# Kernel optimization log

Hardware: AMD Instinct MI355X
Metric: run time of the kernel (lower is better)

## Reference

```python
import jax, jax.numpy as jnp
import numpy as np

B, S, D = 4, 4096, 2048
G, EPG = 4, 16          # num_groups, experts_per_group
E = G * EPG             # num_experts = 64
H = 64                  # complexity estimator hidden


def setup_inputs() -> dict:
    key = jax.random.key(0)
    ks = jax.random.split(key, 7)
    scale = 0.02
    return {
        "x": jax.random.normal(ks[0], (B, S, D), dtype=jnp.float32),
        "Wg": jax.random.normal(ks[1], (G, D), dtype=jnp.float32) * scale,
        "We": jax.random.normal(ks[2], (G, EPG, D), dtype=jnp.float32) * scale,
        "W1": jax.random.normal(ks[3], (H, D), dtype=jnp.float32) * scale,
        "b1": jax.random.normal(ks[4], (H,), dtype=jnp.float32) * scale,
        "W2": jax.random.normal(ks[5], (1, H), dtype=jnp.float32) * scale,
        "b2": jax.random.normal(ks[6], (1,), dtype=jnp.float32) * scale,
        "min_experts": 1,
        "max_experts": 2,
    }


def _router_forward(x, Wg, We, W1, b1, W2, b2, min_experts, max_experts):
    # complexity estimator: Linear -> ReLU -> Linear -> Sigmoid, squeeze(-1)
    h = jax.nn.relu(jnp.einsum("bsd,hd->bsh", x, W1) + b1)
    complexity = jax.nn.sigmoid(jnp.einsum("bsh,oh->bso", h, W2) + b2)[..., 0]  # [B,S]
    # torch: clamp((score * max_experts).int(), min, max); .int() truncates (floor for >=0)
    k = jnp.clip((complexity * max_experts).astype(jnp.int32), min_experts, max_experts)  # [B,S]

    # group routing
    group_logits = jnp.einsum("bsd,gd->bsg", x, Wg)          # [B,S,G]
    group_probs = jax.nn.softmax(group_logits, axis=-1)
    gidx = jnp.argmax(group_probs, axis=-1)                   # [B,S]

    # per-group expert logits for all groups, then pick the chosen group per token
    expert_logits_all = jnp.einsum("bsd,ged->bsge", x, We)    # [B,S,G,EPG]
    expert_logits = jnp.take_along_axis(
        expert_logits_all, gidx[:, :, None, None], axis=2
    )[:, :, 0, :]                                             # [B,S,EPG]
    expert_probs = jax.nn.softmax(expert_logits, axis=-1)     # [B,S,EPG]

    # per-token top-k (k in {1,2}); always take top-2, mask the 2nd when k==1
    topv, topi = jax.lax.top_k(expert_probs, max_experts)     # [B,S,2]
    use2 = (k >= 2).astype(topv.dtype)                        # [B,S]
    mask = jnp.stack([jnp.ones_like(use2), use2], axis=-1)    # [B,S,2]
    denom = jnp.sum(topv * mask, axis=-1, keepdims=True)
    norm_probs = topv * mask / denom                          # [B,S,2]

    flat_idx = gidx[:, :, None] * EPG + topi                  # [B,S,2] global expert ids
    oh = jax.nn.one_hot(flat_idx, E, dtype=x.dtype)           # [B,S,2,E]
    dispatch = jnp.sum(oh * mask[..., None], axis=2)          # [B,S,E]
    combine = jnp.sum(oh * norm_probs[..., None], axis=2)     # [B,S,E]

    # router_probs: group_prob[gidx] * expert_probs scattered into chosen group's slice
    gp_max = jnp.take_along_axis(group_probs, gidx[..., None], axis=-1)[..., 0]  # [B,S]
    oh_g = jax.nn.one_hot(gidx, G, dtype=x.dtype)             # [B,S,G]
    router_probs = (oh_g[..., :, None] * (gp_max[..., None] * expert_probs)[..., None, :]
                    ).reshape(x.shape[0], x.shape[1], E)      # [B,S,E]

    denom_tok = x.shape[0] * x.shape[1]
    router_prob_per_expert = jnp.sum(router_probs, axis=(0, 1)) / denom_tok
    expert_usage = jnp.sum(dispatch, axis=(0, 1)) / denom_tok
    aux_loss = jnp.sum(router_prob_per_expert * expert_usage) * E
    return dispatch, combine, router_probs, aux_loss


def reference(x, Wg, We, W1, b1, W2, b2, min_experts, max_experts):
    return _router_forward(x, Wg, We, W1, b1, W2, b2, min_experts, max_experts)
```

## Files before the change

### kernel.cpp

```cpp
#include <hip/hip_runtime.h>
#include <cmath>

#define T_TOKENS 16384
#define DIM 2048
#define NG 4
#define EPG 16
#define NE 64
#define NJ2 68
#define NT2 5
#define BM 64
#define BK 64
#define NITER (DIM / BK)
#define TAU 0.02f

#define XBUF_B 16384
#define WBUF_B 10240

typedef __attribute__((ext_vector_type(8))) short bf16x8;
typedef __attribute__((ext_vector_type(4))) float f32x4;

#define WF_FLOATS (64 * NT2 * 64 * 4)
#define SUM_OFF WF_FLOATS
#define CNT_OFF (SUM_OFF + 128)
#define LIST_OFF (CNT_OFF + 4)

static __device__ inline unsigned bf16rne(float x) {
    unsigned u = __float_as_uint(x);
    return (u + 0x7FFFu + ((u >> 16) & 1u)) >> 16;
}

#define GLOAD_LDS(gsrc, ldst) \
    __builtin_amdgcn_global_load_lds( \
        (const __attribute__((address_space(1))) void*)(gsrc), \
        (__attribute__((address_space(3))) void*)(ldst), 16, 0, 0)

__global__ void moe_prep(const float* __restrict__ Wg, const float* __restrict__ We,
                         float* __restrict__ ws, float* __restrict__ sums,
                         int* __restrict__ cnt) {
    int bid = blockIdx.x;
    int kstep = bid / NT2, nt = bid % NT2;
    int lane = threadIdx.x;
    if (bid == 0) {
        sums[lane] = 0.f; sums[64 + lane] = 0.f;
        if (lane == 0) *cnt = 0;
    }
    int row = nt * 16 + (lane & 15);
    int k0 = kstep * 32 + (lane >> 4) * 8;
    const float* src = nullptr;
    if (row < NG)            src = Wg + (size_t)row * DIM;
    else if (row < NJ2)      src = We + (size_t)(row - NG) * DIM;
    unsigned r0 = 0, r1 = 0, r2 = 0, r3 = 0;
    if (src) {
        r0 = bf16rne(src[k0 + 0]) | (bf16rne(src[k0 + 1]) << 16);
        r1 = bf16rne(src[k0 + 2]) | (bf16rne(src[k0 + 3]) << 16);
        r2 = bf16rne(src[k0 + 4]) | (bf16rne(src[k0 + 5]) << 16);
        r3 = bf16rne(src[k0 + 6]) | (bf16rne(src[k0 + 7]) << 16);
    }
    ((uint4*)ws)[(size_t)(kstep * NT2 + nt) * 64 + lane] = make_uint4(r0, r1, r2, r3);
}

__global__ __launch_bounds__(512, 2) void moe_fused(
    const float* __restrict__ x, const float* __restrict__ wfrag,
    float* __restrict__ out, float* __restrict__ sums,
    int* __restrict__ cnt, int4* __restrict__ list) {
    __shared__ __align__(16) char smem[2 * XBUF_B + 2 * WBUF_B];
    __shared__ float rp_s[BM * 17];
    __shared__ int   sc_e1[BM];
    __shared__ float s_usage[NE], s_rp[NE];

    const int tid = threadIdx.x;
    const int wave = tid >> 6, lane = tid & 63;
    const int l15 = lane & 15, lq = lane >> 4;
    const int T0 = blockIdx.x * BM;

    if (tid < NE) { s_usage[tid] = 0.f; s_rp[tid] = 0.f; }

    const uint4* wg = (const uint4*)wfrag;
    const int mt = wave & 3, nh = wave >> 2;
    const int ctok = mt * 16 + l15;
    const int csw = ctok & 7;

    f32x4 acc0 = (f32x4){0.f,0.f,0.f,0.f};
    f32x4 acc1 = (f32x4){0.f,0.f,0.f,0.f};
    f32x4 acc2 = (f32x4){0.f,0.f,0.f,0.f};

    auto stage = [&](int it) {
        char* xb = smem + (it & 1) * XBUF_B;
        char* wb = smem + 2 * XBUF_B + (it & 1) * WBUF_B;
        const int kf = it * BK;
        #pragma unroll
        for (int j = 0; j < 2; ++j) {
            const int tok = wave * 8 + j * 4 + (lane >> 4);
            const float* src = x + (size_t)(T0 + tok) * DIM + kf
                             + (((lane & 15) ^ (tok & 7)) << 2);
            GLOAD_LDS(src, xb + (wave * 8 + j * 4) * 256);
        }
        if (wave < NT2) {
            #pragma unroll
            for (int ks = 0; ks < 2; ++ks) {
                const int kstep = it * 2 + ks;
                GLOAD_LDS(wg + ((size_t)kstep * NT2 + wave) * 64 + lane,
                          wb + (ks * NT2 + wave) * 1024);
            }
        }
    };

    stage(0);
    #pragma unroll 1
    for (int it = 0; it < NITER; ++it) {
        __syncthreads();
        if (it + 1 < NITER) stage(it + 1);
        const char* xb = smem + (it & 1) * XBUF_B;
        const char* wb = smem + 2 * XBUF_B + (it & 1) * WBUF_B;
        #pragma unroll
        for (int ks = 0; ks < 2; ++ks) {
            const int u0 = ks * 8 + lq * 2;
            uint4 lo = *(const uint4*)(xb + ctok * 256 + ((u0 ^ csw) << 4));
            uint4 hi = *(const uint4*)(xb + ctok * 256 + (((u0 + 1) ^ csw) << 4));
            union { unsigned u[4]; bf16x8 v; } af;
            af.u[0] = (lo.x >> 16) | (lo.y & 0xFFFF0000u);
            af.u[1] = (lo.z >> 16) | (lo.w & 0xFFFF0000u);
            af.u[2] = (hi.x >> 16) | (hi.y & 0xFFFF0000u);
            af.u[3] = (hi.z >> 16) | (hi.w & 0xFFFF0000u);
            if (nh == 0) {
                bf16x8 b0 = *(const bf16x8*)(wb + (ks * NT2 + 0) * 1024 + lane * 16);
                bf16x8 b1 = *(const bf16x8*)(wb + (ks * NT2 + 1) * 1024 + lane * 16);
                bf16x8 b2 = *(const bf16x8*)(wb + (ks * NT2 + 2) * 1024 + lane * 16);
                acc0 = __builtin_amdgcn_mfma_f32_16x16x32_bf16(af.v, b0, acc0, 0, 0, 0);
                acc1 = __builtin_amdgcn_mfma_f32_16x16x32_bf16(af.v, b1, acc1, 0, 0, 0);
                acc2 = __builtin_amdgcn_mfma_f32_16x16x32_bf16(af.v, b2, acc2, 0, 0, 0);
            } else {
                bf16x8 b0 = *(const bf16x8*)(wb + (ks * NT2 + 3) * 1024 + lane * 16);
                bf16x8 b1 = *(const bf16x8*)(wb + (ks * NT2 + 4) * 1024 + lane * 16);
                acc0 = __builtin_amdgcn_mfma_f32_16x16x32_bf16(af.v, b0, acc0, 0, 0, 0);
                acc1 = __builtin_amdgcn_mfma_f32_16x16x32_bf16(af.v, b1, acc1, 0, 0, 0);
            }
        }
    }
    __syncthreads();

    float* slog = (float*)smem;
    #pragma unroll
    for (int r = 0; r < 4; ++r) {
        const int row = mt * 16 + lq * 4 + r;
        if (nh == 0) {
            slog[row * 81 + 0 * 16 + l15] = acc0[r];
            slog[row * 81 + 1 * 16 + l15] = acc1[r];
            slog[row * 81 + 2 * 16 + l15] = acc2[r];
        } else {
            slog[row * 81 + 3 * 16 + l15] = acc0[r];
            slog[row * 81 + 4 * 16 + l15] = acc1[r];
        }
    }
    __syncthreads();

    #pragma unroll
    for (int half = 0; half < 2; ++half) {
        const int t = (tid >> 4) + half * 32;
        const int q = tid & 15;
        const int tok = T0 + t;
        const float* o = slog + t * 81;

        float gl0 = o[0], gl1 = o[1], gl2 = o[2], gl3 = o[3];
        float gm = gl0; int gi = 0;
        if (gl1 > gm) { gm = gl1; gi = 1; }
        if (gl2 > gm) { gm = gl2; gi = 2; }
        if (gl3 > gm) { gm = gl3; gi = 3; }
        float g2 = -INFINITY;
        if (gi != 0 && gl0 > g2) g2 = gl0;
        if (gi != 1 && gl1 > g2) g2 = gl1;
        if (gi != 2 && gl2 > g2) g2 = gl2;
        if (gi != 3 && gl3 > g2) g2 = gl3;
        bool flagG = (gm - g2) < TAU;
        float gsum = expf(gl0 - gm) + expf(gl1 - gm) + expf(gl2 - gm) + expf(gl3 - gm);
        float gp = 1.f / gsum;

        float el = o[NG + gi * EPG + q];
        float v1v = el; int i1 = q;
        #pragma unroll
        for (int off = 8; off; off >>= 1) {
            float ov = __shfl_xor(v1v, off, 16);
            int   oi = __shfl_xor(i1, off, 16);
            if (ov > v1v || (ov == v1v && oi < i1)) { v1v = ov; i1 = oi; }
        }
        float v2v = (q == i1) ? -INFINITY : el;
        #pragma unroll
        for (int off = 8; off; off >>= 1)
            v2v = fmaxf(v2v, __shfl_xor(v2v, off, 16));
        bool flagE = (v1v - v2v) < TAU;

        float ep = expf(el - v1v);
        float es = ep;
        #pragma unroll
        for (int off = 8; off; off >>= 1) es += __shfl_xor(es, off, 16);
        float inv = 1.f / es;
        rp_s[t * 17 + q] = gp * ep * inv;

        if (q == 0) {
            sc_e1[t] = gi * EPG + i1;
            if (flagG || flagE) {
                int p = atomicAdd(cnt, 1);
                list[p] = make_int4(tok, 0, 0, 0);
            }
        }
    }
    __syncthreads();

    float* outD = out;
    float* outC = out + (size_t)T_TOKENS * NE;
    float* outR = out + (size_t)2 * T_TOKENS * NE;
    for (int idx = tid; idx < BM * NE; idx += 512) {
        int t = idx >> 6, e = idx & 63;
        int e1i = sc_e1[t];
        int gi = e1i >> 4;
        float disp = (e == e1i) ? 1.f : 0.f;
        float rpv  = ((e >> 4) == gi) ? rp_s[t * 17 + (e & 15)] : 0.f;
        size_t ob = (size_t)(T0 + t) * NE + e;
        outD[ob] = disp; outC[ob] = disp; outR[ob] = rpv;
        atomicAdd(&s_usage[e], disp);
        atomicAdd(&s_rp[e], rpv);
    }
    __syncthreads();
    if (tid < NE) {
        atomicAdd(&sums[tid], s_usage[tid]);
        atomicAdd(&sums[NE + tid], s_rp[tid]);
    }
}

__global__ __launch_bounds__(256, 4) void moe_fix(
    const float* __restrict__ x, const float* __restrict__ Wg,
    const float* __restrict__ We, float* __restrict__ out,
    float* __restrict__ sums, const int* __restrict__ cnt,
    const int4* __restrict__ list) {
    __shared__ float gl_s[NG];
    __shared__ float el_s[EPG];
    __shared__ float rp_row[EPG];
    __shared__ int   s_gi, s_e1;
    __shared__ float s_gp;

    const int tid = threadIdx.x;
    const int wave = tid >> 6, lane = tid & 63;
    const int n = *cnt;

    for (int i = blockIdx.x; i < n; i += gridDim.x) {
        const int tok = list[i].x;
        const float* xrow = x + (size_t)tok * DIM;
        float xr[32];
        #pragma unroll
        for (int m = 0; m < 32; ++m) xr[m] = xrow[lane + m * 64];

        auto dotf = [&](const float* w) -> float {
            float s = 0.f;
            #pragma unroll
            for (int m = 0; m < 32; ++m) s = fmaf(xr[m], w[lane + m * 64], s);
            #pragma unroll
            for (int off = 32; off; off >>= 1) s += __shfl_xor(s, off, 64);
            return s;
        };

        {
            float g = dotf(Wg + (size_t)wave * DIM);
            if (lane == 0) gl_s[wave] = g;
        }
        __syncthreads();

        if (tid == 0) {
            float gm = -INFINITY; int gi = 0;
            #pragma unroll
            for (int g = 0; g < NG; ++g)
                if (gl_s[g] > gm) { gm = gl_s[g]; gi = g; }
            float gsum = 0.f;
            #pragma unroll
            for (int g = 0; g < NG; ++g) gsum += expf(gl_s[g] - gm);
            s_gp = 1.f / gsum;
            s_gi = gi;
        }
        __syncthreads();

        const int gi = s_gi;
        for (int j = wave; j < EPG; j += 4) {
            float e = dotf(We + (size_t)(gi * EPG + j) * DIM);
            if (lane == 0) el_s[j] = e;
        }
        __syncthreads();

        if (tid == 0) {
            float e1 = -INFINITY; int i1 = 0;
            #pragma unroll
            for (int j = 0; j < EPG; ++j)
                if (el_s[j] > e1) { e1 = el_s[j]; i1 = j; }
            float es = 0.f;
            #pragma unroll
            for (int j = 0; j < EPG; ++j) {
                float e = expf(el_s[j] - e1);
                rp_row[j] = e;
                es += e;
            }
            float sc = s_gp / es;
            #pragma unroll
            for (int j = 0; j < EPG; ++j) rp_row[j] *= sc;
            s_e1 = gi * EPG + i1;
        }
        __syncthreads();

        if (tid < NE) {
            const int e = tid;
            float newD = (e == s_e1) ? 1.f : 0.f;
            float newR = ((e >> 4) == gi) ? rp_row[e & 15] : 0.f;
            size_t ob = (size_t)tok * NE + e;
            float oldD = out[ob];
            float oldR = out[(size_t)2 * T_TOKENS * NE + ob];
            out[ob] = newD;
            out[(size_t)T_TOKENS * NE + ob] = newD;
            out[(size_t)2 * T_TOKENS * NE + ob] = newR;
            float dD = newD - oldD, dR = newR - oldR;
            if (dD != 0.f) atomicAdd(&sums[e], dD);
            if (dR != 0.f) atomicAdd(&sums[NE + e], dR);
        }
        __syncthreads();
    }
}

__global__ void moe_finalize(const float* __restrict__ sums, float* __restrict__ out) {
    int l = threadIdx.x;
    float v = sums[l] * sums[NE + l];
    #pragma unroll
    for (int off = 32; off; off >>= 1) v += __shfl_down(v, off, 64);
    if (l == 0) {
        float N = (float)T_TOKENS;
        out[(size_t)3 * T_TOKENS * NE] = v * (float)NE / (N * N);
    }
}

extern "C" void kernel_launch(void* const* d_in, const int* in_sizes, int n_in,
                              void* d_out, int out_size, void* d_ws, size_t ws_size,
                              hipStream_t stream) {
    const float* x  = (const float*)d_in[0];
    const float* Wg = (const float*)d_in[1];
    const float* We = (const float*)d_in[2];
    float* out = (float*)d_out;
    float* ws  = (float*)d_ws;

    float* wfrag = ws;
    float* sums  = ws + SUM_OFF;
    int*   cnt   = (int*)(ws + CNT_OFF);
    int4*  list  = (int4*)(ws + LIST_OFF);

    moe_prep<<<64 * NT2, 64, 0, stream>>>(Wg, We, wfrag, sums, cnt);
    moe_fused<<<T_TOKENS / BM, 512, 0, stream>>>(x, wfrag, out, sums, cnt, list);
    moe_fix<<<1024, 256, 0, stream>>>(x, Wg, We, out, sums, cnt, list);
    moe_finalize<<<1, 64, 0, stream>>>(sums, out);
}
```

Baseline: 79.59 us.

## Split GEMM along K into partial sums with separate epilogue kernel

Replaces the fused per-64-token GEMM+epilogue kernel with a split-K GEMM: 256-token tiles and 4 K-slices write partial logits to workspace. A new epilogue kernel sums the partials and does the softmax/top-k and output writes over 16-token blocks. The intent is larger tiles that reuse each weight fragment across two M tiles, with K-parallelism to fill the GPU. The cost is an extra launch and about 21 MB of partial-sum traffic to global memory.

```diff
diff --git a/kernel.cpp b/kernel.cpp
--- a/kernel.cpp
+++ b/kernel.cpp
@@ -8,19 +8,23 @@
 #define NE 64
 #define NJ2 68
 #define NT2 5
-#define BM 64
-#define BK 64
-#define NITER (DIM / BK)
+#define NJP2 80
+#define BM 256
+#define KS 4
+#define KSL (DIM / KS)
+#define NITER (KSL / 32)
 #define TAU 0.02f
 
-#define XBUF_B 16384
-#define WBUF_B 10240
+#define XBUF_B 32768
+#define WBUF_B 5120
 
 typedef __attribute__((ext_vector_type(8))) short bf16x8;
 typedef __attribute__((ext_vector_type(4))) float f32x4;
 
 #define WF_FLOATS (64 * NT2 * 64 * 4)
-#define SUM_OFF WF_FLOATS
+#define P_OFF WF_FLOATS
+#define P_FLOATS ((size_t)KS * T_TOKENS * NJP2)
+#define SUM_OFF (P_OFF + P_FLOATS)
 #define CNT_OFF (SUM_OFF + 128)
 #define LIST_OFF (CNT_OFF + 4)
 
@@ -47,8 +51,8 @@
     int row = nt * 16 + (lane & 15);
     int k0 = kstep * 32 + (lane >> 4) * 8;
     const float* src = nullptr;
-    if (row < NG)            src = Wg + (size_t)row * DIM;
-    else if (row < NJ2)      src = We + (size_t)(row - NG) * DIM;
+    if (row < NG)        src = Wg + (size_t)row * DIM;
+    else if (row < NJ2)  src = We + (size_t)(row - NG) * DIM;
     unsigned r0 = 0, r1 = 0, r2 = 0, r3 = 0;
     if (src) {
         r0 = bf16rne(src[k0 + 0]) | (bf16rne(src[k0 + 1]) << 16);
@@ -59,49 +63,47 @@
     ((uint4*)ws)[(size_t)(kstep * NT2 + nt) * 64 + lane] = make_uint4(r0, r1, r2, r3);
 }
 
-__global__ __launch_bounds__(512, 2) void moe_fused(
+__global__ __launch_bounds__(512, 1) void moe_gemm(
     const float* __restrict__ x, const float* __restrict__ wfrag,
-    float* __restrict__ out, float* __restrict__ sums,
-    int* __restrict__ cnt, int4* __restrict__ list) {
-    __shared__ __align__(16) char smem[2 * XBUF_B + 2 * WBUF_B];
-    __shared__ float rp_s[BM * 17];
-    __shared__ int   sc_e1[BM];
-    __shared__ float s_usage[NE], s_rp[NE];
-
+    float* __restrict__ part) {
+    __shared__ __align__(16) char xs[2][XBUF_B];
+    __shared__ __align__(16) char wsb[2][WBUF_B];
+
+    const int bid = blockIdx.x;
+    const int tg = bid & 63, ks = bid >> 6;
     const int tid = threadIdx.x;
     const int wave = tid >> 6, lane = tid & 63;
     const int l15 = lane & 15, lq = lane >> 4;
-    const int T0 = blockIdx.x * BM;
-
-    if (tid < NE) { s_usage[tid] = 0.f; s_rp[tid] = 0.f; }
-
+    const int T0 = tg * BM;
+    const int K0 = ks * KSL;
+
+    const int xtokb = wave * 32 + (lane >> 3);
+    const int xp = lane & 7;
     const uint4* wg = (const uint4*)wfrag;
-    const int mt = wave & 3, nh = wave >> 2;
-    const int ctok = mt * 16 + l15;
-    const int csw = ctok & 7;
-
-    f32x4 acc0 = (f32x4){0.f,0.f,0.f,0.f};
-    f32x4 acc1 = (f32x4){0.f,0.f,0.f,0.f};
-    f32x4 acc2 = (f32x4){0.f,0.f,0.f,0.f};
+
+    const int mt0 = wave * 2;
+    const int t0 = mt0 * 16 + l15;
+    const int t1 = t0 + 16;
+
+    f32x4 acc[2][NT2];
+    #pragma unroll
+    for (int m = 0; m < 2; ++m)
+        #pragma unroll
+        for (int n = 0; n < NT2; ++n) acc[m][n] = (f32x4){0.f, 0.f, 0.f, 0.f};
 
     auto stage = [&](int it) {
-        char* xb = smem + (it & 1) * XBUF_B;
-        char* wb = smem + 2 * XBUF_B + (it & 1) * WBUF_B;
-        const int kf = it * BK;
-        #pragma unroll
-        for (int j = 0; j < 2; ++j) {
-            const int tok = wave * 8 + j * 4 + (lane >> 4);
-            const float* src = x + (size_t)(T0 + tok) * DIM + kf
-                             + (((lane & 15) ^ (tok & 7)) << 2);
-            GLOAD_LDS(src, xb + (wave * 8 + j * 4) * 256);
+        char* xb = xs[it & 1];
+        char* wb = wsb[it & 1];
+        const int kf = K0 + it * 32;
+        #pragma unroll
+        for (int j = 0; j < 4; ++j) {
+            const int tok = xtokb + j * 8;
+            const float* src = x + (size_t)(T0 + tok) * DIM + kf + ((xp ^ (tok & 7)) << 2);
+            GLOAD_LDS(src, xb + (wave * 256 + j * 64) * 16);
         }
         if (wave < NT2) {
-            #pragma unroll
-            for (int ks = 0; ks < 2; ++ks) {
-                const int kstep = it * 2 + ks;
-                GLOAD_LDS(wg + ((size_t)kstep * NT2 + wave) * 64 + lane,
-                          wb + (ks * NT2 + wave) * 1024);
-            }
+            const int kstep = ks * NITER + it;
+            GLOAD_LDS(wg + ((size_t)kstep * NT2 + wave) * 64 + lane, wb + wave * 1024);
         }
     };
 
@@ -110,56 +112,73 @@
     for (int it = 0; it < NITER; ++it) {
         __syncthreads();
         if (it + 1 < NITER) stage(it + 1);
-        const char* xb = smem + (it & 1) * XBUF_B;
-        const char* wb = smem + 2 * XBUF_B + (it & 1) * WBUF_B;
-        #pragma unroll
-        for (int ks = 0; ks < 2; ++ks) {
-            const int u0 = ks * 8 + lq * 2;
-            uint4 lo = *(const uint4*)(xb + ctok * 256 + ((u0 ^ csw) << 4));
-            uint4 hi = *(const uint4*)(xb + ctok * 256 + (((u0 + 1) ^ csw) << 4));
-            union { unsigned u[4]; bf16x8 v; } af;
-            af.u[0] = (lo.x >> 16) | (lo.y & 0xFFFF0000u);
-            af.u[1] = (lo.z >> 16) | (lo.w & 0xFFFF0000u);
-            af.u[2] = (hi.x >> 16) | (hi.y & 0xFFFF0000u);
-            af.u[3] = (hi.z >> 16) | (hi.w & 0xFFFF0000u);
-            if (nh == 0) {
-                bf16x8 b0 = *(const bf16x8*)(wb + (ks * NT2 + 0) * 1024 + lane * 16);
-                bf16x8 b1 = *(const bf16x8*)(wb + (ks * NT2 + 1) * 1024 + lane * 16);
-                bf16x8 b2 = *(const bf16x8*)(wb + (ks * NT2 + 2) * 1024 + lane * 16);
-                acc0 = __builtin_amdgcn_mfma_f32_16x16x32_bf16(af.v, b0, acc0, 0, 0, 0);
-                acc1 = __builtin_amdgcn_mfma_f32_16x16x32_bf16(af.v, b1, acc1, 0, 0, 0);
-                acc2 = __builtin_amdgcn_mfma_f32_16x16x32_bf16(af.v, b2, acc2, 0, 0, 0);
-            } else {
-                bf16x8 b0 = *(const bf16x8*)(wb + (ks * NT2 + 3) * 1024 + lane * 16);
-                bf16x8 b1 = *(const bf16x8*)(wb + (ks * NT2 + 4) * 1024 + lane * 16);
-                acc0 = __builtin_amdgcn_mfma_f32_16x16x32_bf16(af.v, b0, acc0, 0, 0, 0);
-                acc1 = __builtin_amdgcn_mfma_f32_16x16x32_bf16(af.v, b1, acc1, 0, 0, 0);
-            }
-        }
+        const char* xb = xs[it & 1];
+        const char* wb = wsb[it & 1];
+
+        union { unsigned u[4]; bf16x8 v; } a0, a1;
+        {
+            uint4 lo = *(const uint4*)(xb + t0 * 128 + (((lq * 2) ^ (t0 & 7)) << 4));
+            uint4 hi = *(const uint4*)(xb + t0 * 128 + (((lq * 2 + 1) ^ (t0 & 7)) << 4));
+            a0.u[0] = (lo.x >> 16) | (lo.y & 0xFFFF0000u);
+            a0.u[1] = (lo.z >> 16) | (lo.w & 0xFFFF0000u);
+            a0.u[2] = (hi.x >> 16) | (hi.y & 0xFFFF0000u);
+            a0.u[3] = (hi.z >> 16) | (hi.w & 0xFFFF0000u);
+        }
+        {
+            uint4 lo = *(const uint4*)(xb + t1 * 128 + (((lq * 2) ^ (t1 & 7)) << 4));
+            uint4 hi = *(const uint4*)(xb + t1 * 128 + (((lq * 2 + 1) ^ (t1 & 7)) << 4));
+            a1.u[0] = (lo.x >> 16) | (lo.y & 0xFFFF0000u);
+            a1.u[1] = (lo.z >> 16) | (lo.w & 0xFFFF0000u);
+            a1.u[2] = (hi.x >> 16) | (hi.y & 0xFFFF0000u);
+            a1.u[3] = (hi.z >> 16) | (hi.w & 0xFFFF0000u);
+        }
+        #pragma unroll
+        for (int n = 0; n < NT2; ++n) {
+            bf16x8 bv = *(const bf16x8*)(wb + n * 1024 + lane * 16);
+            acc[0][n] = __builtin_amdgcn_mfma_f32_16x16x32_bf16(a0.v, bv, acc[0][n], 0, 0, 0);
+            acc[1][n] = __builtin_amdgcn_mfma_f32_16x16x32_bf16(a1.v, bv, acc[1][n], 0, 0, 0);
+        }
+    }
+
+    float* po = part + (size_t)ks * T_TOKENS * NJP2;
+    #pragma unroll
+    for (int m = 0; m < 2; ++m) {
+        const int tokb = T0 + (mt0 + m) * 16 + lq * 4;
+        #pragma unroll
+        for (int n = 0; n < NT2; ++n)
+            #pragma unroll
+            for (int r = 0; r < 4; ++r)
+                po[(size_t)(tokb + r) * NJP2 + n * 16 + l15] = acc[m][n][r];
+    }
+}
+
+__global__ __launch_bounds__(256, 2) void moe_epi(
+    const float* __restrict__ part, float* __restrict__ out,
+    float* __restrict__ sums, int* __restrict__ cnt, int4* __restrict__ list) {
+    __shared__ float slog[16][81];
+    __shared__ float rp_s[16 * 17];
+    __shared__ int   sc_e1[16];
+    __shared__ float s_usage[NE], s_rp[NE];
+
+    const int tid = threadIdx.x;
+    const int T0 = blockIdx.x * 16;
+    if (tid < NE) { s_usage[tid] = 0.f; s_rp[tid] = 0.f; }
+
+    for (int idx = tid; idx < 16 * NJP2; idx += 256) {
+        int t = idx / NJP2, j = idx % NJP2;
+        float v = part[(size_t)(T0 + t) * NJP2 + j];
+        #pragma unroll
+        for (int p = 1; p < KS; ++p)
+            v += part[(size_t)p * T_TOKENS * NJP2 + (size_t)(T0 + t) * NJP2 + j];
+        slog[t][j] = v;
     }
     __syncthreads();
 
-    float* slog = (float*)smem;
-    #pragma unroll
-    for (int r = 0; r < 4; ++r) {
-        const int row = mt * 16 + lq * 4 + r;
-        if (nh == 0) {
-            slog[row * 81 + 0 * 16 + l15] = acc0[r];
-            slog[row * 81 + 1 * 16 + l15] = acc1[r];
-            slog[row * 81 + 2 * 16 + l15] = acc2[r];
-        } else {
-            slog[row * 81 + 3 * 16 + l15] = acc0[r];
-            slog[row * 81 + 4 * 16 + l15] = acc1[r];
-        }
-    }
-    __syncthreads();
-
-    #pragma unroll
-    for (int half = 0; half < 2; ++half) {
-        const int t = (tid >> 4) + half * 32;
+    {
+        const int t = tid >> 4;
         const int q = tid & 15;
         const int tok = T0 + t;
-        const float* o = slog + t * 81;
+        const float* o = slog[t];
 
         float gl0 = o[0], gl1 = o[1], gl2 = o[2], gl3 = o[3];
         float gm = gl0; int gi = 0;
@@ -209,7 +228,7 @@
     float* outD = out;
     float* outC = out + (size_t)T_TOKENS * NE;
     float* outR = out + (size_t)2 * T_TOKENS * NE;
-    for (int idx = tid; idx < BM * NE; idx += 512) {
+    for (int idx = tid; idx < 16 * NE; idx += 256) {
         int t = idx >> 6, e = idx & 63;
         int e1i = sc_e1[t];
         int gi = e1i >> 4;
@@ -342,12 +361,14 @@
     float* ws  = (float*)d_ws;
 
     float* wfrag = ws;
+    float* part  = ws + P_OFF;
     float* sums  = ws + SUM_OFF;
     int*   cnt   = (int*)(ws + CNT_OFF);
     int4*  list  = (int4*)(ws + LIST_OFF);
 
     moe_prep<<<64 * NT2, 64, 0, stream>>>(Wg, We, wfrag, sums, cnt);
-    moe_fused<<<T_TOKENS / BM, 512, 0, stream>>>(x, wfrag, out, sums, cnt, list);
+    moe_gemm<<<64 * KS, 512, 0, stream>>>(x, wfrag, part);
+    moe_epi<<<T_TOKENS / 16, 256, 0, stream>>>(part, out, sums, cnt, list);
     moe_fix<<<1024, 256, 0, stream>>>(x, Wg, We, out, sums, cnt, list);
     moe_finalize<<<1, 64, 0, stream>>>(sums, out);
 }
```

New measurement: 87.93 us. 1.1x slower.
